# Kernel optimization log

Hardware: AMD Instinct MI355X
Metric: run time of the kernel (lower is better)

The kernel has to match this reference:

```python
import jax, jax.numpy as jnp
import numpy as np

H = 12            # heads
NB_FEATURES = 256 # Performer random features
EPS = 1e-4        # performer_pytorch softmax_kernel eps


def _gaussian_orthogonal_matrix(nb_rows, nb_cols, rng):
    # performer_pytorch gaussian_orthogonal_random_matrix, scaling=0
    nb_full = nb_rows // nb_cols
    blocks = []
    for _ in range(nb_full):
        q, _ = np.linalg.qr(rng.standard_normal((nb_cols, nb_cols)))
        blocks.append(q.T)
    rem = nb_rows - nb_full * nb_cols
    if rem > 0:
        q, _ = np.linalg.qr(rng.standard_normal((nb_cols, nb_cols)))
        blocks.append(q.T[:rem])
    M = np.concatenate(blocks, axis=0)
    multiplier = np.linalg.norm(rng.standard_normal((nb_rows, nb_cols)), axis=1)
    return (multiplier[:, None] * M).astype(np.float32)


def setup_inputs() -> dict:
    key = jax.random.key(0)
    ks = jax.random.split(key, 10)
    B, N, D = 8, 2048, 768
    s = D ** -0.5  # keep activations O(1) so exp() in FAVOR+ is stable
    inp = {
        "x": jax.random.normal(ks[0], (B, N, D), jnp.float32),
        "Wq": jax.random.normal(ks[1], (D, D), jnp.float32) * s,
        "bq": jnp.zeros((D,), jnp.float32),
        "Wk": jax.random.normal(ks[2], (D, D), jnp.float32) * s,
        "bk": jnp.zeros((D,), jnp.float32),
        "Wv": jax.random.normal(ks[3], (D, D), jnp.float32) * s,
        "bv": jnp.zeros((D,), jnp.float32),
        "Wo": jax.random.normal(ks[4], (D, D), jnp.float32) * s,
        "bo": jnp.zeros((D,), jnp.float32),
        "proj": jnp.asarray(_gaussian_orthogonal_matrix(NB_FEATURES, D // H, np.random.default_rng(0))),
    }
    return inp


def _softmax_kernel(x, proj, is_query):
    # x: [b,h,n,d], proj: [m,d] -> phi(x): [b,h,n,m]
    d = x.shape[-1]
    data_normalizer = d ** -0.25
    ratio = proj.shape[0] ** -0.5
    xp = jnp.einsum('bhnd,md->bhnm', x * data_normalizer, proj)
    diag = jnp.sum(x * x, axis=-1, keepdims=True) * 0.5 * (data_normalizer ** 2)
    if is_query:
        m = jax.lax.stop_gradient(jnp.max(xp, axis=-1, keepdims=True))
    else:
        m = jax.lax.stop_gradient(jnp.max(xp, axis=(-1, -2), keepdims=True))
    return ratio * (jnp.exp(xp - diag - m) + EPS)


def reference(x, Wq, bq, Wk, bk, Wv, bv, Wo, bo, proj):
    b, n, dim = x.shape
    d = dim // H
    # qkv projections, split into heads: [b,h,n,d]
    q = (x @ Wq.T + bq).reshape(b, n, H, d).transpose(0, 2, 1, 3)
    k = (x @ Wk.T + bk).reshape(b, n, H, d).transpose(0, 2, 1, 3)
    v = (x @ Wv.T + bv).reshape(b, n, H, d).transpose(0, 2, 1, 3)
    # FAVOR+ feature maps: [b,h,n,m]
    qp = _softmax_kernel(q, proj, True)
    kp = _softmax_kernel(k, proj, False)
    # non-causal linear attention
    k_sum = kp.sum(axis=2)                                  # [b,h,m]
    D_inv = 1.0 / jnp.einsum('bhnm,bhm->bhn', qp, k_sum)    # [b,h,n]
    ctx = jnp.einsum('bhnm,bhnd->bhmd', kp, v)              # [b,h,m,d]
    out = jnp.einsum('bhmd,bhnm,bhn->bhnd', ctx, qp, D_inv)
    out = out.transpose(0, 2, 1, 3).reshape(b, n, dim)
    return out @ Wo.T + bo
```

## Files before the change

### kernel.cpp

```cpp
#include <hip/hip_runtime.h>
#include <stdint.h>

typedef unsigned short u16;
typedef unsigned int u32;
typedef __attribute__((ext_vector_type(8))) short short8;
typedef __attribute__((ext_vector_type(4))) float floatx4;

#define HN 12
#define DH 64
#define DM 768
#define NS 2048
#define NB 8
#define MF 256
#define BN (NB*NS)
#define BH (NB*HN)

#define NRM 0.35355339059327373f
#define RATIO 0.0625f
#define EPSV 1e-4f

__device__ __forceinline__ float b2f(u32 u){ union{u32 i; float f;} x; x.i=u<<16; return x.f; }
__device__ __forceinline__ u32 f2b(float v){ union{float f; u32 u;} x; x.f=v; return (x.u + 0x7FFFu + ((x.u>>16)&1u))>>16; }
__device__ __forceinline__ u32 fkey(float v){ union{float f; u32 u;} x; x.f=v; return (x.u&0x80000000u)? ~x.u : (x.u|0x80000000u); }
__device__ __forceinline__ float funkey(u32 k){ union{u32 u; float f;} x; x.u=(k&0x80000000u)? (k^0x80000000u) : ~k; return x.f; }
__device__ __forceinline__ void bld8(uint4 r, float s, float* f){
  f[0]=b2f(r.x&0xffffu)*s; f[1]=b2f(r.x>>16)*s;
  f[2]=b2f(r.y&0xffffu)*s; f[3]=b2f(r.y>>16)*s;
  f[4]=b2f(r.z&0xffffu)*s; f[5]=b2f(r.z>>16)*s;
  f[6]=b2f(r.w&0xffffu)*s; f[7]=b2f(r.w>>16)*s;
}
__device__ __forceinline__ void load8(const void* base, size_t idx, int isf32, float s, float* f){
  if(isf32){
    const float* p=(const float*)base + idx;
    const float4 u=((const float4*)p)[0], v=((const float4*)p)[1];
    f[0]=u.x*s; f[1]=u.y*s; f[2]=u.z*s; f[3]=u.w*s;
    f[4]=v.x*s; f[5]=v.y*s; f[6]=v.z*s; f[7]=v.w*s;
  }else{
    uint4 r=*(const uint4*)((const u16*)base+idx);
    bld8(r,s,f);
  }
}
__device__ __forceinline__ float ld1(const void* base, int idx, int isf32){
  return isf32 ? ((const float*)base)[idx] : b2f((u32)((const u16*)base)[idx]);
}
__device__ __forceinline__ void gl16(const void* g, void* l){
  __builtin_amdgcn_global_load_lds(
    (const __attribute__((address_space(1))) u32*)g,
    (__attribute__((address_space(3))) u32*)l, 16, 0, 0);
}

__global__ __launch_bounds__(64) void k_detect(const u16* __restrict__ x, int* __restrict__ flag)
{
  __shared__ int w[64], z[64];
  const int t=threadIdx.x;
  int wild=0, zero=0;
  for(int i=t;i<256;i+=64){
    u32 u=(u32)x[2*i];
    u32 e=(u>>7)&0xFFu;
    if(e>=0x90u) wild++;
    if((u&0x7FFFu)==0u) zero++;
  }
  w[t]=wild; z[t]=zero; __syncthreads();
  if(t==0){
    int W=0,Z=0;
    for(int i=0;i<64;++i){W+=w[i];Z+=z[i];}
    flag[0]=(W>16||Z>200)?1:0;
  }
}

__global__ __launch_bounds__(256) void k_cvtw(const void* __restrict__ Wq,
    const void* __restrict__ Wk, const void* __restrict__ Wv, const void* __restrict__ Wo,
    u16* __restrict__ wb, u16* __restrict__ wob, const int* __restrict__ flagp)
{
  const int isf32=*flagp;
  const size_t WSZ=(size_t)DM*DM;
  size_t idx=((size_t)blockIdx.x*256+threadIdx.x)*8;
  const void* src; size_t off; u16* dst;
  if(idx<3*WSZ){ int w=(int)(idx/WSZ); src=(w==0)?Wq:((w==1)?Wk:Wv); off=idx-(size_t)w*WSZ; dst=wb+idx; }
  else { src=Wo; off=idx-3*WSZ; dst=wob+off; }
  if(isf32){
    const float* p=(const float*)src+off;
    float4 u=((const float4*)p)[0], v=((const float4*)p)[1];
    uint4 st;
    st.x=f2b(u.x)|(f2b(u.y)<<16); st.y=f2b(u.z)|(f2b(u.w)<<16);
    st.z=f2b(v.x)|(f2b(v.y)<<16); st.w=f2b(v.z)|(f2b(v.w)<<16);
    *(uint4*)dst=st;
  }else{
    *(uint4*)dst=*(const uint4*)((const u16*)src+off);
  }
}

__global__ __launch_bounds__(256) void k_cvtp(const void* __restrict__ proj,
    u16* __restrict__ pn, const int* __restrict__ flagp)
{
  const int isf32=*flagp;
  const size_t idx=((size_t)blockIdx.x*256+threadIdx.x)*8;
  float pf[8];
  load8(proj, idx, isf32, NRM, pf);
  uint4 st;
  st.x=f2b(pf[0])|(f2b(pf[1])<<16); st.y=f2b(pf[2])|(f2b(pf[3])<<16);
  st.z=f2b(pf[4])|(f2b(pf[5])<<16); st.w=f2b(pf[6])|(f2b(pf[7])<<16);
  *(uint4*)(pn+idx)=st;
}

__global__ __launch_bounds__(256) void k_cvtx(const void* __restrict__ x,
    u16* __restrict__ xb, const int* __restrict__ flagp)
{
  const int isf32=*flagp;
  const size_t idx=((size_t)blockIdx.x*256+threadIdx.x)*8;
  float f[8];
  load8(x, idx, isf32, 1.0f, f);
  uint4 st;
  st.x=f2b(f[0])|(f2b(f[1])<<16); st.y=f2b(f[2])|(f2b(f[3])<<16);
  st.z=f2b(f[4])|(f2b(f[5])<<16); st.w=f2b(f[6])|(f2b(f[7])<<16);
  *(uint4*)(xb+idx)=st;
}

__global__ __launch_bounds__(256) void k_diag(const u16* __restrict__ src, float* __restrict__ dk)
{
  const size_t row=(size_t)blockIdx.x*256+threadIdx.x;
  const u16* p=src+row*DH;
  float s=0.f;
#pragma unroll
  for(int c=0;c<DH;c+=8){
    uint4 r=*(const uint4*)(p+c);
    float f[8]; bld8(r,1.0f,f);
#pragma unroll
    for(int j=0;j<8;++j) s+=f[j]*f[j];
  }
  dk[row]=0.5f*NRM*NRM*s;
}

__device__ __forceinline__ void gemm_epilogue(const floatx4 acc[4][4], int mode, int oflag,
    int m0, int n0, int l, int wr4, int wc4,
    const void* bias0, const void* bias1, const void* bias2,
    u16* q, u16* k, u16* v, void* outv)
{
  const int rbase=(l>>4)*4, cl=l&15;
  if(mode==0){
    const int which=n0/DM;
    const void* bias=(which==0)?bias0:((which==1)?bias1:bias2);
    u16* outp=(which==0)?q:((which==1)?k:v);
    const int cb=n0-which*DM;
#pragma unroll
    for(int j=0;j<4;++j){
      const int col=cb+(wc4+j)*16+cl;
      const int h=col>>6, dd=col&63;
      const float bb=ld1(bias,col,oflag);
#pragma unroll
      for(int i=0;i<4;++i){
#pragma unroll
        for(int r=0;r<4;++r){
          const int grow=m0+(wr4+i)*16+rbase+r;
          const int b_=grow>>11, n=grow&2047;
          const u16 val=(u16)f2b(acc[i][j][r]+bb);
          if(which==2) outp[((size_t)(b_*HN+h)*DH+dd)*NS + n]=val;
          else         outp[((size_t)((b_*HN+h)*NS+n))*DH + dd]=val;
        }
      }
    }
  }else{
#pragma unroll
    for(int j=0;j<4;++j){
      const int col=n0+(wc4+j)*16+cl;
      const float bb=ld1(bias0,col,oflag);
#pragma unroll
      for(int i=0;i<4;++i){
#pragma unroll
        for(int r=0;r<4;++r){
          const int grow=m0+(wr4+i)*16+rbase+r;
          const float val=acc[i][j][r]+bb;
          if(oflag) ((float*)outv)[(size_t)grow*DM+col]=val;
          else      ((u16*)outv)[(size_t)grow*DM+col]=(u16)f2b(val);
        }
      }
    }
  }
}

__global__ __launch_bounds__(256) void k_gemm2(const u16* __restrict__ A16,
    const u16* __restrict__ B16,
    const void* __restrict__ bias0, const void* __restrict__ bias1, const void* __restrict__ bias2,
    u16* __restrict__ q, u16* __restrict__ k, u16* __restrict__ v,
    void* __restrict__ outv, const int* __restrict__ flagp, const int mode)
{
  __shared__ short At[16*512];
  __shared__ short Bt[16*512];
  const int oflag=*flagp;
  const int t=threadIdx.x, l=t&63, w=t>>6;
  const int m0=blockIdx.x*128, n0=blockIdx.y*128;
  const int wr4=(w>>1)*4, wc4=(w&1)*4;
  const int srow=l&15, skg=l>>4;
  floatx4 acc[4][4]={};
  for(int k0=0;k0<DM;k0+=64){
    __syncthreads();
#pragma unroll
    for(int s=0;s<4;++s){
      const int bi=w*4+s, rb=bi>>1, kh=bi&1;
      const int kc=k0+kh*32+skg*8;
      gl16(A16 + (size_t)(m0+rb*16+srow)*DM + kc, &At[bi*512]);
      gl16(B16 + (size_t)(n0+rb*16+srow)*DM + kc, &Bt[bi*512]);
    }
    __syncthreads();
#pragma unroll
    for(int kh=0;kh<2;++kh){
      short8 af[4], bf[4];
#pragma unroll
      for(int i=0;i<4;++i) af[i]=*(short8*)&At[((wr4+i)*2+kh)*512+l*8];
#pragma unroll
      for(int j=0;j<4;++j) bf[j]=*(short8*)&Bt[((wc4+j)*2+kh)*512+l*8];
#pragma unroll
      for(int i=0;i<4;++i)
#pragma unroll
        for(int j=0;j<4;++j)
          acc[i][j]=__builtin_amdgcn_mfma_f32_16x16x32_bf16(af[i],bf[j],acc[i][j],0,0,0);
    }
  }
  gemm_epilogue(acc,mode,oflag,m0,n0,l,wr4,wc4,bias0,bias1,bias2,q,k,v,outv);
}

__global__ __launch_bounds__(256) void k_gemm_f(const void* __restrict__ Araw,
    const u16* __restrict__ B16,
    const void* __restrict__ bias0, const void* __restrict__ bias1, const void* __restrict__ bias2,
    u16* __restrict__ q, u16* __restrict__ k, u16* __restrict__ v,
    void* __restrict__ outv, const int* __restrict__ flagp, const int mode)
{
  __shared__ short At[16*512];
  __shared__ short Bt[16*512];
  const int oflag=*flagp;
  const int isf32=(mode==0)?oflag:0;
  const int t=threadIdx.x, l=t&63, w=t>>6;
  const int m0=blockIdx.x*128, n0=blockIdx.y*128;
  const int wr4=(w>>1)*4, wc4=(w&1)*4;
  const int srow=l&15, skg=l>>4;
  floatx4 acc[4][4]={};
  for(int k0=0;k0<DM;k0+=64){
    __syncthreads();
#pragma unroll
    for(int s=0;s<4;++s){
      const int bi=w*4+s, rb=bi>>1, kh=bi&1;
      const int kc=k0+kh*32+skg*8;
      uint4 va;
      if(isf32){
        const float* ap=(const float*)Araw + (size_t)(m0+rb*16+srow)*DM + kc;
        float4 u=((const float4*)ap)[0], vv=((const float4*)ap)[1];
        va.x=f2b(u.x)|(f2b(u.y)<<16);  va.y=f2b(u.z)|(f2b(u.w)<<16);
        va.z=f2b(vv.x)|(f2b(vv.y)<<16); va.w=f2b(vv.z)|(f2b(vv.w)<<16);
      }else{
        va=*(const uint4*)((const u16*)Araw + (size_t)(m0+rb*16+srow)*DM + kc);
      }
      const uint4 vb=*(const uint4*)(B16 + (size_t)(n0+rb*16+srow)*DM + kc);
      *(uint4*)&At[bi*512+l*8]=va;
      *(uint4*)&Bt[bi*512+l*8]=vb;
    }
    __syncthreads();
#pragma unroll
    for(int kh=0;kh<2;++kh){
      short8 af[4], bf[4];
#pragma unroll
      for(int i=0;i<4;++i) af[i]=*(short8*)&At[((wr4+i)*2+kh)*512+l*8];
#pragma unroll
      for(int j=0;j<4;++j) bf[j]=*(short8*)&Bt[((wc4+j)*2+kh)*512+l*8];
#pragma unroll
      for(int i=0;i<4;++i)
#pragma unroll
        for(int j=0;j<4;++j)
          acc[i][j]=__builtin_amdgcn_mfma_f32_16x16x32_bf16(af[i],bf[j],acc[i][j],0,0,0);
    }
  }
  gemm_epilogue(acc,mode,oflag,m0,n0,l,wr4,wc4,bias0,bias1,bias2,q,k,v,outv);
}

#define SBOFF(slot,kh,mf) ((((slot)*32)+((kh)*16)+(mf))*512)
#define STA(kt,kh) do{ \
  const int o_=SBOFF((kt)&1,(kh),0); \
  const size_t g_=(size_t)(kt)*64+(size_t)(kh)*32; \
  gl16(Ar0+g_, &As[o_+w*512]); \
  gl16(Ar0+(size_t)128*768+g_, &As[o_+(8+w)*512]); \
}while(0)
#define STB(kt,kh) do{ \
  const int o_=SBOFF((kt)&1,(kh),0); \
  const size_t g_=(size_t)(kt)*64+(size_t)(kh)*32; \
  gl16(Br0+g_, &Bs[o_+w*512]); \
  gl16(Br0+(size_t)128*768+g_, &Bs[o_+(8+w)*512]); \
}while(0)
#define LDA8(kt,kh) do{ const int o_=SBOFF((kt)&1,(kh),wr*8)+l*8; \
  _Pragma("unroll") for(int i_=0;i_<8;++i_) a[i_]=*(short8*)&As[o_+i_*512]; }while(0)
#define LDB2(kt,kh,np) do{ const int o_=SBOFF((kt)&1,(kh),wc*4+(np)*2)+l*8; \
  b[0]=*(short8*)&Bs[o_]; b[1]=*(short8*)&Bs[o_+512]; }while(0)
#define MM(np) do{ _Pragma("unroll") for(int i_=0;i_<8;++i_){ \
  acc[i_][(np)*2+0]=__builtin_amdgcn_mfma_f32_16x16x32_bf16(a[i_],b[0],acc[i_][(np)*2+0],0,0,0); \
  acc[i_][(np)*2+1]=__builtin_amdgcn_mfma_f32_16x16x32_bf16(a[i_],b[1],acc[i_][(np)*2+1],0,0,0); } }while(0)
#define FEN asm volatile("" ::: "memory")
#define BARR do{ FEN; __builtin_amdgcn_s_barrier(); FEN; }while(0)
#define WV8 asm volatile("s_waitcnt vmcnt(8)" ::: "memory")
#define WV4 asm volatile("s_waitcnt vmcnt(4)" ::: "memory")
#define WV0 asm volatile("s_waitcnt vmcnt(0)" ::: "memory")
#define WL0 do{ asm volatile("s_waitcnt lgkmcnt(0)" ::: "memory"); __builtin_amdgcn_sched_barrier(0); }while(0)
#define PH_O(kt,kh,SST) do{ LDA8(kt,kh); LDB2(kt,kh,0); SST; BARR; WL0; \
  __builtin_amdgcn_s_setprio(1); MM(0); __builtin_amdgcn_s_setprio(0); BARR; }while(0)
#define PH_E(kt,kh,SST,WST) do{ LDB2(kt,kh,1); SST; WST; BARR; WL0; \
  __builtin_amdgcn_s_setprio(1); MM(1); __builtin_amdgcn_s_setprio(0); BARR; }while(0)

__global__ __launch_bounds__(512,2) void k_gemm8(const u16* __restrict__ A16,
    const u16* __restrict__ B16,
    const void* __restrict__ bias0, const void* __restrict__ bias1, const void* __restrict__ bias2,
    u16* __restrict__ q, u16* __restrict__ k, u16* __restrict__ v,
    void* __restrict__ outv, const int* __restrict__ flagp, const int mode,
    float* __restrict__ dq_, float* __restrict__ dk_)
{
  __shared__ short As[2*2*16*512];
  __shared__ short Bs[2*2*16*512];
  const int oflag=*flagp;
  const int t=threadIdx.x, l=t&63, w=t>>6;
  const int wr=w>>2, wc=w&3;
  const int lrow=l&15, lk8=(l>>4)*8;
  int bid = blockIdx.y*gridDim.x + blockIdx.x;
  const int nwg = gridDim.x*gridDim.y;
  const int nN  = gridDim.y;
  bid = (bid&7)*(nwg>>3) + (bid>>3);
  const int mi = bid/nN;
  const int m0 = mi*256;
  const int n0 = (bid - mi*nN)*256;

  const u16* Ar0 = A16 + (size_t)(m0 + w*16 + lrow)*768 + lk8;
  const u16* Br0 = B16 + (size_t)(n0 + w*16 + lrow)*768 + lk8;
  floatx4 acc[8][4]={};
  short8 a[8], b[2];

  STA(0,0); STB(0,0); STA(0,1); STB(0,1); STA(1,0); STB(1,0);
  WV8; BARR;

  for(int i=0;i<5;++i){
    const int kt=2*i;
    PH_O(kt,0,   STA(kt+1,1));
    PH_E(kt,0,   STB(kt+1,1), WV8);
    PH_O(kt,1,   STA(kt+2,0));
    PH_E(kt,1,   STB(kt+2,0), WV8);
    PH_O(kt+1,0, STA(kt+2,1));
    PH_E(kt+1,0, STB(kt+2,1), WV8);
    PH_O(kt+1,1, STA(kt+3,0));
    PH_E(kt+1,1, STB(kt+3,0), WV8);
  }
  PH_O(10,0, STA(11,1));
  PH_E(10,0, STB(11,1), WV8);
  PH_O(10,1, (void)0);
  PH_E(10,1, (void)0, WV4);
  PH_O(11,0, (void)0);
  PH_E(11,0, (void)0, WV0);
  PH_O(11,1, (void)0);
  PH_E(11,1, (void)0, (void)0);

  const int cl=l&15, q4=l>>4;
  if(mode==0){
    const int which=n0/DM;
    const int cb0=n0-which*DM;
    const void* bias=(which==0)?bias0:((which==1)?bias1:bias2);
    u16* outp=(which==0)?q:((which==1)?k:v);
    if(which==2){
#pragma unroll
      for(int j=0;j<4;++j){
        const int col=wc*64+j*16+cl;
        const float bb=ld1(bias,cb0+col,oflag);
        char* cbase=(char*)((col<128)? (void*)(As+col*256) : (void*)(Bs+(col-128)*256));
        const int X=(col&7)<<4;
#pragma unroll
        for(int i=0;i<8;++i){
          const int rowb=wr*128+i*16+q4*4;
          uint2 pk;
          pk.x=f2b(acc[i][j][0]+bb)|(f2b(acc[i][j][1]+bb)<<16);
          pk.y=f2b(acc[i][j][2]+bb)|(f2b(acc[i][j][3]+bb)<<16);
          *(uint2*)(cbase + ((rowb*2)^X)) = pk;
        }
      }
      __syncthreads();
      const int b_=m0>>11, nbase=m0&2047;
#pragma unroll
      for(int tt=0;tt<16;++tt){
        const int task=tt*8+w;
        const int colg=task>>2, qq=task&3;
        const int col=colg*8+(l>>3), sub=l&7;
        char* cbase=(char*)((col<128)? (void*)(As+col*256) : (void*)(Bs+(col-128)*256));
        const uint4 d4=*(const uint4*)(cbase + ((qq*128+sub*16)^((col&7)<<4)));
        const int gcol=cb0+col, h=gcol>>6, dd=gcol&63;
        const int n=nbase+qq*64+sub*8;
        *(uint4*)&outp[((size_t)(b_*HN+h)*DH+dd)*NS + n]=d4;
      }
    } else {
      float bb4[4];
#pragma unroll
      for(int j=0;j<4;++j) bb4[j]=ld1(bias, cb0+wc*64+j*16+cl, oflag);
      float* dptr=(which==0)? dq_ : dk_;
#pragma unroll
      for(int i=0;i<8;++i){
#pragma unroll
        for(int r=0;r<4;++r){
          const int row=wr*128+i*16+q4*4+r;
          char* rbase=(char*)((row<128)? (void*)(As+row*256) : (void*)(Bs+(row-128)*256));
          const int X=(row&3)<<4;
          float s=0.f;
#pragma unroll
          for(int j=0;j<4;++j){
            const int col=wc*64+j*16+cl;
            const u16 hv=(u16)f2b(acc[i][j][r]+bb4[j]);
            *(u16*)(rbase + ((col*2)^X)) = hv;
            const float fv=b2f(hv);
            s+=fv*fv;
          }
          s+=__shfl_xor(s,1,64); s+=__shfl_xor(s,2,64);
          s+=__shfl_xor(s,4,64); s+=__shfl_xor(s,8,64);
          if(cl==0){
            const int grow=m0+row, b_=grow>>11, n=grow&2047;
            dptr[(size_t)(b_*HN + (cb0>>6)+wc)*NS + n]=0.5f*NRM*NRM*s;
          }
        }
      }
      __syncthreads();
      const int hb=cb0>>6;
#pragma unroll
      for(int tt=0;tt<16;++tt){
        const int task=tt*8+w;
        const int rowg=task>>2, qq=task&3;
        const int row=rowg*8+(l>>3), sub=l&7;
        char* rbase=(char*)((row<128)? (void*)(As+row*256) : (void*)(Bs+(row-128)*256));
        const uint4 d4=*(const uint4*)(rbase + ((qq*128+sub*16)^((row&3)<<4)));
        const int grow=m0+row, b_=grow>>11, n=grow&2047;
        *(uint4*)&outp[((size_t)(b_*HN+hb+qq)*NS+n)*DH + sub*8]=d4;
      }
    }
  } else {
    if(oflag){
#pragma unroll
      for(int p=0;p<2;++p){
        if(wr==p){
#pragma unroll
          for(int j=0;j<4;++j){
            const int col=wc*64+j*16+cl;
            const float bb=ld1(bias0,n0+col,oflag);
#pragma unroll
            for(int i=0;i<8;++i){
#pragma unroll
              for(int r=0;r<4;++r){
                const int row=i*16+q4*4+r;
                char* rbase=(char*)((row<64)? (void*)(As+row*512) : (void*)(Bs+(row-64)*512));
                *(float*)(rbase + ((col*4)^((row&3)<<4))) = acc[i][j][r]+bb;
              }
            }
          }
        }
        __syncthreads();
#pragma unroll
        for(int tt=0;tt<16;++tt){
          const int task=tt*8+w;
          const int rowg=task>>3, qq=task&7;
          const int row=rowg*8+(l>>3), sub=l&7;
          char* rbase=(char*)((row<64)? (void*)(As+row*512) : (void*)(Bs+(row-64)*512));
          const uint4 d4=*(const uint4*)(rbase + ((qq*128+sub*16)^((row&3)<<4)));
          const size_t grow=(size_t)m0+p*128+row;
          *(uint4*)((char*)outv + (grow*DM+n0)*4 + qq*128 + sub*16)=d4;
        }
        __syncthreads();
      }
    } else {
#pragma unroll
      for(int j=0;j<4;++j){
        const int col=wc*64+j*16+cl;
        const float bb=ld1(bias0,n0+col,oflag);
#pragma unroll
        for(int i=0;i<8;++i){
#pragma unroll
          for(int r=0;r<4;++r){
            const int row=wr*128+i*16+q4*4+r;
            char* rbase=(char*)((row<128)? (void*)(As+row*256) : (void*)(Bs+(row-128)*256));
            *(u16*)(rbase + ((col*2)^((row&3)<<4))) = (u16)f2b(acc[i][j][r]+bb);
          }
        }
      }
      __syncthreads();
#pragma unroll
      for(int tt=0;tt<16;++tt){
        const int task=tt*8+w;
        const int rowg=task>>2, qq=task&3;
        const int row=rowg*8+(l>>3), sub=l&7;
        char* rbase=(char*)((row<128)? (void*)(As+row*256) : (void*)(Bs+(row-128)*256));
        const uint4 d4=*(const uint4*)(rbase + ((qq*128+sub*16)^((row&3)<<4)));
        const int grow=m0+row;
        *(uint4*)((u16*)outv + (size_t)grow*DM + n0 + qq*64 + sub*8)=d4;
      }
    }
  }
}

__global__ __launch_bounds__(256) void k_xpk2(const u16* __restrict__ kb,
    const u16* __restrict__ pn, u32* __restrict__ kmax)
{
  __shared__ short Bt[32*512];
  __shared__ short At[8*512];
  __shared__ float red[256];
  const int t=threadIdx.x, l=t&63, w=t>>6;
  const int bh=blockIdx.y, nb0=blockIdx.x*256;
  for(int s=t;s<2048;s+=256){
    const int ub=s>>6, l2=s&63, mt=ub>>1, kh=ub&1;
    const int row=mt*16+(l2&15), kc=kh*32+(l2>>4)*8;
    *(uint4*)&Bt[ub*512+l2*8]=*(const uint4*)(pn + (size_t)row*DH + kc);
  }
  float vmax=-3.4e38f;
  for(int c=0;c<4;++c){
    const int n0=nb0+c*64;
    __syncthreads();
    for(int s=t;s<512;s+=256){
      const int ua=s>>6, l2=s&63, rb=ua>>1, kh=ua&1;
      const int n=n0+rb*16+(l2&15), kc=kh*32+(l2>>4)*8;
      *(uint4*)&At[ua*512+l2*8]=*(const uint4*)(kb + ((size_t)bh*NS+n)*DH + kc);
    }
    __syncthreads();
    const short8 af0=*(short8*)&At[(w*2+0)*512+l*8];
    const short8 af1=*(short8*)&At[(w*2+1)*512+l*8];
#pragma unroll
    for(int mt=0;mt<16;++mt){
      floatx4 a={};
      a=__builtin_amdgcn_mfma_f32_16x16x32_bf16(af0,*(short8*)&Bt[(mt*2+0)*512+l*8],a,0,0,0);
      a=__builtin_amdgcn_mfma_f32_16x16x32_bf16(af1,*(short8*)&Bt[(mt*2+1)*512+l*8],a,0,0,0);
      vmax=fmaxf(vmax,fmaxf(fmaxf(a[0],a[1]),fmaxf(a[2],a[3])));
    }
  }
  red[t]=vmax; __syncthreads();
  for(int s=128;s>0;s>>=1){ if(t<s) red[t]=fmaxf(red[t],red[t+s]); __syncthreads(); }
  if(t==0) atomicMax(kmax+bh, fkey(red[0]));
}

__global__ __launch_bounds__(256) void k_ctx2(const u16* __restrict__ kb,
    const u16* __restrict__ vT, const u16* __restrict__ pn,
    const float* __restrict__ dkbuf, const u32* __restrict__ kmax,
    float* __restrict__ ctxT, float* __restrict__ ksum)
{
  __shared__ short Bt[32*512];
  __shared__ u16   Ks[256*72];
  __shared__ short AtV[8*512];
  __shared__ float dg[64];
  const int t=threadIdx.x, l=t&63, w=t>>6;
  const int split=blockIdx.x, bh=blockIdx.y;
  for(int s=t;s<2048;s+=256){
    const int ub=s>>6, l2=s&63, mt=ub>>1, kh=ub&1;
    const int row=mt*16+(l2&15), kc=kh*32+(l2>>4)*8;
    *(uint4*)&Bt[ub*512+l2*8]=*(const uint4*)(pn + (size_t)row*DH + kc);
  }
  const float kM=funkey(kmax[bh]);
  float ksr=0.f;
  floatx4 acc2[4][4]={};
  for(int c=0;c<8;++c){
    const int n0=split*512+c*64;
    __syncthreads();
    for(int s=t;s<512;s+=256){
      const int ua=s>>6, l2=s&63, rb=ua>>1, kh=ua&1;
      const int n=n0+rb*16+(l2&15), kc=kh*32+(l2>>4)*8;
      *(uint4*)&AtV[ua*512+l2*8]=*(const uint4*)(kb + ((size_t)bh*NS+n)*DH + kc);
    }
    if(t<64) dg[t]=dkbuf[(size_t)bh*NS+n0+t];
    __syncthreads();
    short8 af[4][2];
#pragma unroll
    for(int rb=0;rb<4;++rb){
      af[rb][0]=*(short8*)&AtV[(rb*2+0)*512+l*8];
      af[rb][1]=*(short8*)&AtV[(rb*2+1)*512+l*8];
    }
    float dgl[16];
#pragma unroll
    for(int rb=0;rb<4;++rb)
#pragma unroll
      for(int r=0;r<4;++r) dgl[rb*4+r]=dg[rb*16+(l>>4)*4+r];
#pragma unroll
    for(int ml=0;ml<4;++ml){
      const int mt=w*4+ml;
      const short8 bf0=*(short8*)&Bt[(mt*2+0)*512+l*8];
      const short8 bf1=*(short8*)&Bt[(mt*2+1)*512+l*8];
      const int m=mt*16+(l&15);
#pragma unroll
      for(int rb=0;rb<4;++rb){
        floatx4 a={};
        a=__builtin_amdgcn_mfma_f32_16x16x32_bf16(af[rb][0],bf0,a,0,0,0);
        a=__builtin_amdgcn_mfma_f32_16x16x32_bf16(af[rb][1],bf1,a,0,0,0);
        const int nb=rb*16+(l>>4)*4;
        const float v0=RATIO*(__expf(a[0]-dgl[rb*4+0]-kM)+EPSV);
        const float v1=RATIO*(__expf(a[1]-dgl[rb*4+1]-kM)+EPSV);
        const float v2=RATIO*(__expf(a[2]-dgl[rb*4+2]-kM)+EPSV);
        const float v3=RATIO*(__expf(a[3]-dgl[rb*4+3]-kM)+EPSV);
        *(u32*)&Ks[m*72+nb]  =f2b(v0)|(f2b(v1)<<16);
        *(u32*)&Ks[m*72+nb+2]=f2b(v2)|(f2b(v3)<<16);
      }
    }
    __syncthreads();
    for(int s=t;s<512;s+=256){
      const int uv=s>>6, l2=s&63, dt=uv>>1, kh=uv&1;
      const int d=dt*16+(l2&15), nn=n0+kh*32+(l2>>4)*8;
      *(uint4*)&AtV[uv*512+l2*8]=*(const uint4*)(vT + ((size_t)bh*DH+d)*NS + nn);
    }
    {
      float s8=0.f;
#pragma unroll
      for(int j=0;j<8;++j){
        const uint4 kk=*(const uint4*)&Ks[t*72+j*8];
        s8+=b2f(kk.x&0xffffu)+b2f(kk.x>>16)+b2f(kk.y&0xffffu)+b2f(kk.y>>16)
           +b2f(kk.z&0xffffu)+b2f(kk.z>>16)+b2f(kk.w&0xffffu)+b2f(kk.w>>16);
      }
      ksr+=s8;
    }
    __syncthreads();
#pragma unroll
    for(int i=0;i<4;++i){
      const int row=(w*4+i)*16+(l&15);
      const short8 a0=*(short8*)&Ks[row*72 + 0*32+(l>>4)*8];
      const short8 a1=*(short8*)&Ks[row*72 + 1*32+(l>>4)*8];
#pragma unroll
      for(int dt=0;dt<4;++dt){
        acc2[i][dt]=__builtin_amdgcn_mfma_f32_16x16x32_bf16(a0,*(short8*)&AtV[(dt*2+0)*512+l*8],acc2[i][dt],0,0,0);
        acc2[i][dt]=__builtin_amdgcn_mfma_f32_16x16x32_bf16(a1,*(short8*)&AtV[(dt*2+1)*512+l*8],acc2[i][dt],0,0,0);
      }
    }
  }
#pragma unroll
  for(int i=0;i<4;++i){
#pragma unroll
    for(int dt=0;dt<4;++dt){
#pragma unroll
      for(int r=0;r<4;++r){
        const int m=(w*4+i)*16+(l>>4)*4+r;
        const int d=dt*16+(l&15);
        atomicAdd(&ctxT[((size_t)bh*DH+d)*MF+m], acc2[i][dt][r]);
      }
    }
  }
  atomicAdd(ksum+bh*MF+t, ksr);
}

__global__ __launch_bounds__(256) void k_csplit(const float* __restrict__ ctxT,
    u16* __restrict__ chi, u16* __restrict__ clo, float* __restrict__ ecs)
{
  __shared__ float cred[256];
  const int bh=blockIdx.x, t=threadIdx.x;
  const int d=t>>2, part=t&3;
  const size_t base=((size_t)bh*DH+d)*MF + part*64;
  const float* src=ctxT + base;
  u16* ph=chi + base;
  u16* pl=clo + base;
  float cs=0.f;
  for(int m=0;m<64;m+=4){
    float4 v=*(const float4*)(src+m);
    float vv[4]={v.x,v.y,v.z,v.w};
    u32 h_[4], l_[4];
#pragma unroll
    for(int j=0;j<4;++j){
      cs+=vv[j];
      u32 hh=f2b(vv[j]);
      float rr=vv[j]-b2f(hh);
      h_[j]=hh; l_[j]=f2b(rr);
    }
    uint2 sh, sl;
    sh.x=h_[0]|(h_[1]<<16); sh.y=h_[2]|(h_[3]<<16);
    sl.x=l_[0]|(l_[1]<<16); sl.y=l_[2]|(l_[3]<<16);
    *(uint2*)(ph+m)=sh; *(uint2*)(pl+m)=sl;
  }
  cred[t]=cs; __syncthreads();
  if(part==0) ecs[bh*64+d]=EPSV*(cred[t]+cred[t+1]+cred[t+2]+cred[t+3]);
}

__global__ __launch_bounds__(256) void k_attn2(const u16* __restrict__ qb,
    const u16* __restrict__ pn, const float* __restrict__ dqbuf,
    const float* __restrict__ ksum, const u16* __restrict__ chi, const u16* __restrict__ clo,
    const float* __restrict__ ecs, u16* __restrict__ attn)
{
  __shared__ short At[8*512];
  __shared__ u16 Qf[32*512];
  __shared__ float ksums[256];
  __shared__ float dq_s[64];
  __shared__ float mxs[4][64];
  __shared__ float s1s[4][64];
  __shared__ float a_s[64], dinv_s[64], ec_s[64];
  __shared__ float red4[4];
  __shared__ float epkss;
  const int t=threadIdx.x, l=t&63, w=t>>6;
  const int bh=blockIdx.y, nb0=blockIdx.x*256;
  const int b_=bh/HN, h=bh%HN;
  {
    float kv=ksum[bh*MF+t];
    ksums[t]=kv;
    if(t<64) ec_s[t]=ecs[bh*64+t];
    float s=kv;
#pragma unroll
    for(int o=1;o<64;o<<=1) s+=__shfl_xor(s,o,64);
    if(l==0) red4[w]=s;
  }
  __syncthreads();
  if(t==0) epkss=EPSV*(red4[0]+red4[1]+red4[2]+red4[3]);
  short8 bhf[8], blf[8];
  {
    const int d=w*16+(l&15);
    const size_t base=((size_t)bh*DH+d)*MF;
#pragma unroll
    for(int kc=0;kc<8;++kc){
      const size_t off=base + kc*32+(l>>4)*8;
      bhf[kc]=*(const short8*)(chi+off);
      blf[kc]=*(const short8*)(clo+off);
    }
  }
  for(int c=0;c<4;++c){
    const int n0c=nb0+c*64;
    __syncthreads();
    for(int s=t;s<512;s+=256){
      const int ua=s>>6, l2=s&63, nt=ua>>1, kh=ua&1;
      const int n=n0c+nt*16+(l2&15), kc=kh*32+(l2>>4)*8;
      *(uint4*)&At[ua*512+l2*8]=*(const uint4*)(qb + ((size_t)bh*NS+n)*DH + kc);
    }
    if(t<64) dq_s[t]=dqbuf[(size_t)bh*NS+n0c+t];
    __syncthreads();
    float mxl[4]={-3.4e38f,-3.4e38f,-3.4e38f,-3.4e38f};
    float s1l[4]={0.f,0.f,0.f,0.f};
#pragma unroll
    for(int mt=0;mt<4;++mt){
      const int gm=w*4+mt;
      const u16* pr=pn + ((gm*16+(l&15))<<6) + (l>>4)*8;
      const short8 a0=*(const short8*)(pr);
      const short8 a1=*(const short8*)(pr+32);
      float k4[4];
#pragma unroll
      for(int r=0;r<4;++r) k4[r]=ksums[gm*16+(l>>4)*4+r];
      const int mbase=(gm&1)*16+(l>>4)*4;
      const int lane2=((mbase>>3)*16+(l&15))*8 + (mbase&7);
#pragma unroll
      for(int nt=0;nt<4;++nt){
        floatx4 xp={};
        xp=__builtin_amdgcn_mfma_f32_16x16x32_bf16(a0,*(short8*)&At[(nt*2+0)*512+l*8],xp,0,0,0);
        xp=__builtin_amdgcn_mfma_f32_16x16x32_bf16(a1,*(short8*)&At[(nt*2+1)*512+l*8],xp,0,0,0);
        const float dq=dq_s[nt*16+(l&15)];
        float ev[4];
#pragma unroll
        for(int r=0;r<4;++r){
          const float xv=xp[r];
          mxl[nt]=fmaxf(mxl[nt],xv);
          ev[r]=__expf(xv-dq);
          s1l[nt]+=ev[r]*k4[r];
        }
        u16* qp_=&Qf[(nt*8+(gm>>1))*512 + lane2];
        *(u32*)qp_    =f2b(ev[0])|(f2b(ev[1])<<16);
        *(u32*)(qp_+2)=f2b(ev[2])|(f2b(ev[3])<<16);
      }
    }
#pragma unroll
    for(int nt=0;nt<4;++nt){
      float m_=mxl[nt], s_=s1l[nt];
      m_=fmaxf(m_,__shfl_xor(m_,16,64)); s_+=__shfl_xor(s_,16,64);
      m_=fmaxf(m_,__shfl_xor(m_,32,64)); s_+=__shfl_xor(s_,32,64);
      if(l<16){ mxs[w][nt*16+l]=m_; s1s[w][nt*16+l]=s_; }
    }
    __syncthreads();
    if(t<64){
      float m_=fmaxf(fmaxf(mxs[0][t],mxs[1][t]),fmaxf(mxs[2][t],mxs[3][t]));
      float s_=s1s[0][t]+s1s[1][t]+s1s[2][t]+s1s[3][t];
      float a=__expf(-m_);
      a_s[t]=a;
      dinv_s[t]=1.0f/(a*s_+epkss);
    }
    __syncthreads();
    const int d=w*16+(l&15);
    const float ec=ec_s[d];
#pragma unroll
    for(int nt=0;nt<4;++nt){
      floatx4 y={};
#pragma unroll
      for(int kc=0;kc<8;++kc){
        const short8 e=*(short8*)&Qf[(nt*8+kc)*512+l*8];
        y=__builtin_amdgcn_mfma_f32_16x16x32_bf16(e,bhf[kc],y,0,0,0);
        y=__builtin_amdgcn_mfma_f32_16x16x32_bf16(e,blf[kc],y,0,0,0);
      }
#pragma unroll
      for(int r=0;r<4;++r){
        const int nl=nt*16+(l>>4)*4+r;
        const float val=(a_s[nl]*y[r]+ec)*dinv_s[nl];
        attn[((size_t)(b_*NS+n0c+nl))*DM + h*DH + d]=(u16)f2b(val);
      }
    }
  }
}

extern "C" void kernel_launch(void* const* d_in, const int* in_sizes, int n_in,
                              void* d_out, int out_size, void* d_ws, size_t ws_size,
                              hipStream_t stream)
{
  (void)in_sizes; (void)n_in; (void)out_size;
  const void* x =d_in[0];
  const void* Wq=d_in[1]; const void* bq=d_in[2];
  const void* Wk=d_in[3]; const void* bk=d_in[4];
  const void* Wv=d_in[5]; const void* bv=d_in[6];
  const void* Wo=d_in[7]; const void* bo=d_in[8];
  const void* proj=d_in[9];

  char* ws=(char*)d_ws;
  const size_t SZ=(size_t)BN*DM*2;
  const size_t AUXSZ=19030528;
  const bool big = ws_size >= 4*SZ + AUXSZ;
  u16*   qb  =(u16*)(ws);
  u16*   kb  =(u16*)(ws+SZ);
  u16*   vb  =(u16*)(ws+2*SZ);
  u16*   xb  =(u16*)(ws+3*SZ);
  char*  aux = big ? (ws+4*SZ) : (ws+3*SZ);
  u16*   wb   =(u16*)(aux);
  u16*   wob  =(u16*)(aux+3538944);
  float* ctxT =(float*)(aux+4718592);
  float* ksum =(float*)(aux+11010048);
  u32*   kmax =(u32*)(aux+11108352);
  int*   flag =(int*)(aux+11108736);
  float* dk   =(float*)(aux+11108864);
  float* dqq  =(float*)(aux+11895296);
  u16*   pn   =(u16*)(aux+12681728);
  u16*   chi  =(u16*)(aux+12714496);
  u16*   clo  =(u16*)(aux+15860224);
  float* ecs  =(float*)(aux+19005952);
  u16*   attnb = big ? xb : kb;

  k_detect<<<1,64,0,stream>>>((const u16*)x, flag);
  hipMemsetAsync(ctxT, 0, 6291456+98304+384, stream);
  k_cvtw <<<1152, 256, 0, stream>>>(Wq,Wk,Wv,Wo,wb,wob,flag);
  k_cvtp <<<8, 256, 0, stream>>>(proj, pn, flag);
  if(big){
    k_cvtx <<<(BN*DM)/2048, 256, 0, stream>>>(x, xb, flag);
    k_gemm8<<<dim3(BN/256,2304/256), 512, 0, stream>>>(xb, wb, bq,bk,bv, qb,kb,vb, nullptr, flag, 0, dqq, dk);
  }else{
    k_gemm_f<<<dim3(BN/128,2304/128), 256, 0, stream>>>(x, wb, bq,bk,bv, qb,kb,vb, nullptr, flag, 0);
    k_diag <<<(BH*NS)/256, 256, 0, stream>>>(kb, dk);
    k_diag <<<(BH*NS)/256, 256, 0, stream>>>(qb, dqq);
  }
  k_xpk2 <<<dim3(NS/256,BH), 256, 0, stream>>>(kb, pn, kmax);
  k_ctx2 <<<dim3(4,BH), 256, 0, stream>>>(kb, vb, pn, dk, kmax, ctxT, ksum);
  k_csplit<<<BH, 256, 0, stream>>>(ctxT, chi, clo, ecs);
  k_attn2<<<dim3(NS/256,BH), 256, 0, stream>>>(qb, pn, dqq, ksum, chi, clo, ecs, attnb);
  if(big){
    k_gemm8<<<dim3(BN/256,DM/256), 512, 0, stream>>>(attnb, wob, bo,bo,bo, nullptr,nullptr,nullptr, d_out, flag, 1, nullptr, nullptr);
  }else{
    k_gemm2<<<dim3(BN/128,DM/128), 256, 0, stream>>>(attnb, wob, bo,bo,bo, nullptr,nullptr,nullptr, d_out, flag, 1);
  }
}
```

Before: 489.9 us.

## Replace atomic context accumulation with per-split partial buffers and reduction kernel

On the big-workspace path, the key-feature/value context kernel now writes per-split partial context and key-sum buffers with plain coalesced stores through an LDS transpose, rather than issuing scattered float atomicAdds into a zeroed buffer. A new reduction kernel sums the four partials, produces the bf16 hi/lo split and the eps column sums, and writes the final key sum. This drops the large memset and the atomic traffic, and spreads the split/reduce work over four times as many blocks. In exchange it adds an extra partial-buffer round trip through global memory, and it assumes vb holds V in transposed layout on this path, reusing xb as scratch.

```diff
diff --git a/kernel.cpp b/kernel.cpp
--- a/kernel.cpp
+++ b/kernel.cpp
@@ -633,6 +633,147 @@
   atomicAdd(ksum+bh*MF+t, ksr);
 }
 
+__global__ __launch_bounds__(256,2) void k_ctx3(const u16* __restrict__ kb,
+    const u16* __restrict__ vT, const u16* __restrict__ pn,
+    const float* __restrict__ dkbuf, const u32* __restrict__ kmax,
+    float* __restrict__ ctxP, float* __restrict__ ksumP)
+{
+  __shared__ __align__(16) char SM[66048];
+  short* Ks=(short*)SM;
+  short* Kb=(short*)(SM+32768);
+  short* Vb=(short*)(SM+49152);
+  float* dgb=(float*)(SM+65536);
+  const int t=threadIdx.x, l=t&63, w=t>>6;
+  const int split=blockIdx.x, bh=blockIdx.y;
+  const int n00=split*512;
+  const int lrow=l&15, lk8=(l>>4)*8;
+  const u16* kbase = kb + (size_t)bh*NS*DH;
+  const u16* vbase = vT + (size_t)bh*DH*NS;
+  short8 bf[4][2];
+#pragma unroll
+  for(int ml=0;ml<4;++ml)
+#pragma unroll
+    for(int kh=0;kh<2;++kh)
+      bf[ml][kh]=*(const short8*)(pn + (size_t)((w*4+ml)*16+lrow)*DH + kh*32 + lk8);
+  const float kM=funkey(kmax[bh]);
+  {
+#pragma unroll
+    for(int p=0;p<2;++p){
+      const int u=w+4*p, rb=u>>1, kh=u&1;
+      gl16(kbase + (size_t)(n00+rb*16+lrow)*DH + kh*32+lk8, &Kb[u*512]);
+    }
+#pragma unroll
+    for(int p=0;p<2;++p){
+      const int u=w+4*p, dt=u>>1, kh=u&1;
+      gl16(vbase + (size_t)(dt*16+lrow)*NS + n00+kh*32+lk8, &Vb[u*512]);
+    }
+    if(t<64) dgb[t]=dkbuf[(size_t)bh*NS+n00+t];
+  }
+  __syncthreads();
+  float ksr=0.f;
+  floatx4 acc2[4][4]={};
+  for(int c=0;c<8;++c){
+    const int cur=c&1, nxt=cur^1;
+    if(c<7){
+      const int n1=n00+(c+1)*64;
+#pragma unroll
+      for(int p=0;p<2;++p){
+        const int u=w+4*p, rb=u>>1, kh=u&1;
+        gl16(kbase + (size_t)(n1+rb*16+lrow)*DH + kh*32+lk8, &Kb[nxt*4096+u*512]);
+      }
+#pragma unroll
+      for(int p=0;p<2;++p){
+        const int u=w+4*p, dt=u>>1, kh=u&1;
+        gl16(vbase + (size_t)(dt*16+lrow)*NS + n1+kh*32+lk8, &Vb[nxt*4096+u*512]);
+      }
+    }
+    float dgnv=0.f;
+    if(c<7 && t<64) dgnv=dkbuf[(size_t)bh*NS+n00+(c+1)*64+t];
+    short8 af[4][2];
+#pragma unroll
+    for(int rb=0;rb<4;++rb){
+      af[rb][0]=*(short8*)&Kb[cur*4096+(rb*2+0)*512+l*8];
+      af[rb][1]=*(short8*)&Kb[cur*4096+(rb*2+1)*512+l*8];
+    }
+    float dgl[16];
+#pragma unroll
+    for(int rb=0;rb<4;++rb){
+      const float4 dv=*(const float4*)&dgb[cur*64+rb*16+(l>>4)*4];
+      dgl[rb*4+0]=dv.x; dgl[rb*4+1]=dv.y; dgl[rb*4+2]=dv.z; dgl[rb*4+3]=dv.w;
+    }
+#pragma unroll
+    for(int ml=0;ml<4;++ml){
+      const int m=(w*4+ml)*16+lrow;
+      char* krow=(char*)Ks + m*128;
+      const int xr=(m&7)<<4;
+#pragma unroll
+      for(int rb=0;rb<4;++rb){
+        floatx4 a={};
+        a=__builtin_amdgcn_mfma_f32_16x16x32_bf16(af[rb][0],bf[ml][0],a,0,0,0);
+        a=__builtin_amdgcn_mfma_f32_16x16x32_bf16(af[rb][1],bf[ml][1],a,0,0,0);
+        const float v0=RATIO*(__expf(a[0]-dgl[rb*4+0]-kM)+EPSV);
+        const float v1=RATIO*(__expf(a[1]-dgl[rb*4+1]-kM)+EPSV);
+        const float v2=RATIO*(__expf(a[2]-dgl[rb*4+2]-kM)+EPSV);
+        const float v3=RATIO*(__expf(a[3]-dgl[rb*4+3]-kM)+EPSV);
+        const int nb=rb*16+(l>>4)*4;
+        const u32 bo=((u32)(nb*2)) ^ xr;
+        *(u32*)(krow+bo)  =f2b(v0)|(f2b(v1)<<16);
+        *(u32*)(krow+bo+4)=f2b(v2)|(f2b(v3)<<16);
+      }
+    }
+    __syncthreads();
+    {
+      char* krow=(char*)Ks + t*128;
+      const int xr=(t&7)<<4;
+      float s8=0.f;
+#pragma unroll
+      for(int j=0;j<8;++j){
+        const uint4 kk=*(const uint4*)(krow + ((j*16)^xr));
+        s8+=b2f(kk.x&0xffffu)+b2f(kk.x>>16)+b2f(kk.y&0xffffu)+b2f(kk.y>>16)
+           +b2f(kk.z&0xffffu)+b2f(kk.z>>16)+b2f(kk.w&0xffffu)+b2f(kk.w>>16);
+      }
+      ksr+=s8;
+    }
+#pragma unroll
+    for(int i=0;i<4;++i){
+      const int row=(w*4+i)*16+lrow;
+      char* krow=(char*)Ks + row*128;
+      const int xr=(row&7)<<4;
+      const short8 a0=*(short8*)(krow + (((l>>4)*16)^xr));
+      const short8 a1=*(short8*)(krow + ((64+(l>>4)*16)^xr));
+#pragma unroll
+      for(int dt=0;dt<4;++dt){
+        acc2[i][dt]=__builtin_amdgcn_mfma_f32_16x16x32_bf16(a0,*(short8*)&Vb[cur*4096+(dt*2+0)*512+l*8],acc2[i][dt],0,0,0);
+        acc2[i][dt]=__builtin_amdgcn_mfma_f32_16x16x32_bf16(a1,*(short8*)&Vb[cur*4096+(dt*2+1)*512+l*8],acc2[i][dt],0,0,0);
+      }
+    }
+    if(c<7 && t<64) dgb[nxt*64+t]=dgnv;
+    __syncthreads();
+  }
+  {
+    float* OUT=(float*)SM;
+#pragma unroll
+    for(int i=0;i<4;++i){
+      const int mb=(w*4+i)*16+(l>>4)*4;
+#pragma unroll
+      for(int dt=0;dt<4;++dt){
+        const int d=dt*16+lrow;
+        float4 o; o.x=acc2[i][dt][0]; o.y=acc2[i][dt][1]; o.z=acc2[i][dt][2]; o.w=acc2[i][dt][3];
+        *(float4*)((char*)OUT + d*1024 + ((mb*4)^((d&15)<<4))) = o;
+      }
+    }
+    __syncthreads();
+    float* gout = ctxP + (size_t)(split*BH+bh)*64*256;
+#pragma unroll
+    for(int s=0;s<16;++s){
+      const int d=s*4+w;
+      const uint4 o4=*(const uint4*)((char*)OUT + d*1024 + ((l*16)^((d&15)<<4)));
+      *(uint4*)(gout + (size_t)d*256 + l*4)=o4;
+    }
+    ksumP[(size_t)(split*BH+bh)*256 + t]=ksr;
+  }
+}
+
 __global__ __launch_bounds__(256) void k_csplit(const float* __restrict__ ctxT,
     u16* __restrict__ chi, u16* __restrict__ clo, float* __restrict__ ecs)
 {
@@ -662,6 +803,39 @@
   }
   cred[t]=cs; __syncthreads();
   if(part==0) ecs[bh*64+d]=EPSV*(cred[t]+cred[t+1]+cred[t+2]+cred[t+3]);
+}
+
+__global__ __launch_bounds__(256) void k_csplit3(const float* __restrict__ ctxP,
+    const float* __restrict__ ksumP,
+    u16* __restrict__ chi, u16* __restrict__ clo, float* __restrict__ ecs,
+    float* __restrict__ ksum)
+{
+  __shared__ float wred[16][4];
+  const int bh=blockIdx.y, dq=blockIdx.x;
+  const int t=threadIdx.x, l=t&63, w=t>>6;
+  if(dq==0){
+    float kv=0.f;
+#pragma unroll
+    for(int s=0;s<4;++s) kv+=ksumP[(size_t)(s*BH+bh)*256+t];
+    ksum[bh*MF+t]=kv;
+  }
+#pragma unroll
+  for(int d16=0;d16<16;++d16){
+    const int d=dq*16+d16;
+    float v=0.f;
+#pragma unroll
+    for(int s=0;s<4;++s) v+=ctxP[((size_t)(s*BH+bh)*64+d)*256+t];
+    const u32 hh=f2b(v);
+    const float rr=v-b2f(hh);
+    const size_t ob=((size_t)bh*DH+d)*MF+t;
+    chi[ob]=(u16)hh; clo[ob]=(u16)f2b(rr);
+    float s_=v;
+    s_+=__shfl_xor(s_,1,64); s_+=__shfl_xor(s_,2,64); s_+=__shfl_xor(s_,4,64);
+    s_+=__shfl_xor(s_,8,64); s_+=__shfl_xor(s_,16,64); s_+=__shfl_xor(s_,32,64);
+    if(l==0) wred[d16][w]=s_;
+  }
+  __syncthreads();
+  if(t<16) ecs[bh*64+dq*16+t]=EPSV*(wred[t][0]+wred[t][1]+wred[t][2]+wred[t][3]);
 }
 
 __global__ __launch_bounds__(256) void k_attn2(const u16* __restrict__ qb,
@@ -818,7 +992,8 @@
   u16*   attnb = big ? xb : kb;
 
   k_detect<<<1,64,0,stream>>>((const u16*)x, flag);
-  hipMemsetAsync(ctxT, 0, 6291456+98304+384, stream);
+  if(big) hipMemsetAsync(kmax, 0, 384, stream);
+  else    hipMemsetAsync(ctxT, 0, 6291456+98304+384, stream);
   k_cvtw <<<1152, 256, 0, stream>>>(Wq,Wk,Wv,Wo,wb,wob,flag);
   k_cvtp <<<8, 256, 0, stream>>>(proj, pn, flag);
   if(big){
@@ -830,8 +1005,15 @@
     k_diag <<<(BH*NS)/256, 256, 0, stream>>>(qb, dqq);
   }
   k_xpk2 <<<dim3(NS/256,BH), 256, 0, stream>>>(kb, pn, kmax);
-  k_ctx2 <<<dim3(4,BH), 256, 0, stream>>>(kb, vb, pn, dk, kmax, ctxT, ksum);
-  k_csplit<<<BH, 256, 0, stream>>>(ctxT, chi, clo, ecs);
+  if(big){
+    float* ctxP =(float*)xb;
+    float* ksumP=ctxT;
+    k_ctx3 <<<dim3(4,BH), 256, 0, stream>>>(kb, vb, pn, dk, kmax, ctxP, ksumP);
+    k_csplit3<<<dim3(4,BH), 256, 0, stream>>>(ctxP, ksumP, chi, clo, ecs, ksum);
+  }else{
+    k_ctx2 <<<dim3(4,BH), 256, 0, stream>>>(kb, vb, pn, dk, kmax, ctxT, ksum);
+    k_csplit<<<BH, 256, 0, stream>>>(ctxT, chi, clo, ecs);
+  }
   k_attn2<<<dim3(NS/256,BH), 256, 0, stream>>>(qb, pn, dqq, ksum, chi, clo, ecs, attnb);
   if(big){
     k_gemm8<<<dim3(BN/256,DM/256), 512, 0, stream>>>(attnb, wob, bo,bo,bo, nullptr,nullptr,nullptr, d_out, flag, 1, nullptr, nullptr);
```

Measured after the change: 415.4 us. -15.2%, faster.
